# Performance work log

Measured on AMD Instinct MI355X. Metric: run time of the kernel, lower is better.

## Reference

```python
import jax, jax.numpy as jnp
import numpy as np


def setup_inputs() -> dict:
    key = jax.random.key(0)
    k1, k2, k3 = jax.random.split(key, 3)
    B, D, C = 512, 256, 1000
    embedding = jax.random.normal(k1, (B, D), dtype=jnp.float32)
    labels = jax.random.randint(k2, (B,), 0, C, dtype=jnp.int64)
    W = jax.random.normal(k3, (C, D), dtype=jnp.float32) * 0.02
    return {"embedding": embedding, "labels": labels, "W": W}


def reference(embedding, labels, W):
    # MRL-E loss: (1/D) * sum_{k=1..D} CE(z[:, :k] @ W[:, :k].T, y)
    # Computed incrementally: logits_k = logits_{k-1} + z[:, k] outer W[:, k],
    # which is mathematically identical to recomputing the prefix matmul.
    B, D = embedding.shape
    C = W.shape[0]
    rows = jnp.arange(B)
    labels = labels.astype(jnp.int32)

    def step(logits, cols):
        z_col, w_col = cols  # [B], [C]
        logits = logits + z_col[:, None] * w_col[None, :]  # rank-1 update, [B, C]
        # stable cross-entropy: mean(logsumexp(logits) - logits[i, y_i])
        lse = jax.nn.logsumexp(logits, axis=-1)  # [B]
        lab_logit = logits[rows, labels]  # [B]
        loss_k = jnp.mean(lse - lab_logit)
        return logits, loss_k

    init = jnp.zeros((B, C), dtype=embedding.dtype)
    _, losses = jax.lax.scan(step, init, (embedding.T, W.T))  # losses: [D]
    return jnp.sum(losses) / D
```

## Files before the change

### kernel.cpp

```cpp
#include <hip/hip_runtime.h>
#include <hip/hip_bf16.h>
#include <math.h>


#define MRLE_B 512
#define MRLE_D 256
#define MRLE_C 1000
#define MRLE_CP 1024
#define MRLE_KROWS 264
#define MRLE_NT 256
#define LOG2E 1.4426950408889634f
#define LN2   0.6931471805599453f

#if __has_builtin(__builtin_amdgcn_exp2f)
#define EXP2(x) __builtin_amdgcn_exp2f(x)
#else
#define EXP2(x) __builtin_exp2f(x)
#endif

__global__ __launch_bounds__(256) void mrle_transpose(
    const float* __restrict__ W, unsigned short* __restrict__ Wtb)
{
    __shared__ float tile[64][65];
    const int c0 = blockIdx.x * 64;
    const int k0 = blockIdx.y * 64;
    const int t  = threadIdx.x;
    const int r  = t >> 2;
    const int q  = t & 3;

#pragma unroll
    for (int j = 0; j < 4; ++j) {
        const int c    = c0 + r;
        const int kcol = q * 4 + j * 16;
        float4 v = make_float4(0.f, 0.f, 0.f, 0.f);
        if (c < MRLE_C) v = *(const float4*)&W[(size_t)c * MRLE_D + k0 + kcol];
        tile[r][kcol + 0] = v.x;
        tile[r][kcol + 1] = v.y;
        tile[r][kcol + 2] = v.z;
        tile[r][kcol + 3] = v.w;
    }
    __syncthreads();

#pragma unroll
    for (int j = 0; j < 4; ++j) {
        const int cc = q * 4 + j * 16;
        unsigned short hh[4];
#pragma unroll
        for (int e = 0; e < 4; ++e) {
            const float f = tile[cc + e][r] * LOG2E;
            unsigned int u = __float_as_uint(f);
            u = (u + 0x7FFFu + ((u >> 16) & 1u)) >> 16;
            hh[e] = (unsigned short)u;
        }
        *(ushort4*)&Wtb[(size_t)(k0 + r) * MRLE_CP + c0 + cc] =
            make_ushort4(hh[0], hh[1], hh[2], hh[3]);
    }
}

__global__ __launch_bounds__(MRLE_NT) void mrle_main(
    const float* __restrict__ z,
    const int* __restrict__ labels,
    const float* __restrict__ W,
    const unsigned short* __restrict__ Wtb,
    float* __restrict__ out)
{
    __shared__ float zsh[MRLE_D];
    __shared__ float red[4 * 16 * 64];
    __shared__ float Sw[4 * MRLE_D];
    __shared__ float wred[4];

    const int i  = blockIdx.x;
    const int t  = threadIdx.x;
    const int wv = t >> 6;
    const int l  = t & 63;

    zsh[t] = z[i * MRLE_D + t];
    __syncthreads();

    const float ninf = (t < 250) ? 0.f : -INFINITY;
    float l0 = ninf, l1 = ninf, l2 = ninf, l3 = ninf;

    const uint2* Wp2 = (const uint2*)Wtb + t;

    uint2 wbuf[8];
#pragma unroll
    for (int q = 0; q < 8; ++q) wbuf[q] = Wp2[q * (MRLE_CP / 4)];

    float* redw = red + wv * (16 * 64);
    const int khat = l & 15;
    const int q16  = l & 48;

#pragma unroll 1
    for (int cb = 0; cb < 16; ++cb) {
#pragma unroll
        for (int kk = 0; kk < 16; ++kk) {
            const int k = cb * 16 + kk;
            const uint2 w = wbuf[kk & 7];
            const float zk = zsh[k];
            const float w0 = __uint_as_float(w.x << 16);
            const float w1 = __uint_as_float(w.x & 0xFFFF0000u);
            const float w2 = __uint_as_float(w.y << 16);
            const float w3 = __uint_as_float(w.y & 0xFFFF0000u);
            l0 = fmaf(zk, w0, l0);
            l1 = fmaf(zk, w1, l1);
            l2 = fmaf(zk, w2, l2);
            l3 = fmaf(zk, w3, l3);
            redw[kk * 64 + ((l + kk) & 63)] =
                (EXP2(l0) + EXP2(l1)) + (EXP2(l2) + EXP2(l3));
            wbuf[kk & 7] = Wp2[(k + 8) * (MRLE_CP / 4)];
        }

        float s = 0.f;
#pragma unroll
        for (int u = 0; u < 16; ++u)
            s += redw[khat * 64 + ((q16 + u + khat) & 63)];
        s += __shfl_xor(s, 16);
        s += __shfl_xor(s, 32);
        if (l < 16) Sw[wv * MRLE_D + cb * 16 + khat] = s;
    }

    __syncthreads();

    const float S = (Sw[t] + Sw[MRLE_D + t]) +
                    (Sw[2 * MRLE_D + t] + Sw[3 * MRLE_D + t]);
    const float lse2 = __log2f(S);

    const int y = labels[i];
    const float lab = zsh[t] * W[(size_t)y * MRLE_D + t] * (float)(MRLE_D - t);

    float v = lse2 * LN2 - lab;
#pragma unroll
    for (int d = 1; d < 64; d <<= 1) v += __shfl_xor(v, d);
    if (l == 0) wred[wv] = v;
    __syncthreads();
    if (t == 0)
        atomicAdd(out, (wred[0] + wred[1] + wred[2] + wred[3]) *
                           (1.0f / ((float)MRLE_B * (float)MRLE_D)));
}

extern "C" void kernel_launch(void* const* d_in, const int* in_sizes, int n_in,
                              void* d_out, int out_size, void* d_ws, size_t ws_size,
                              hipStream_t stream) {
    const float* z      = (const float*)d_in[0];
    const int*   labels = (const int*)d_in[1];
    const float* W      = (const float*)d_in[2];
    float*       out    = (float*)d_out;

    unsigned short* Wtb = (unsigned short*)d_ws;

    hipMemsetAsync(out, 0, sizeof(float), stream);
    mrle_transpose<<<dim3(16, 4), 256, 0, stream>>>(W, Wtb);
    mrle_main<<<MRLE_B, MRLE_NT, 0, stream>>>(z, labels, W, Wtb, out);
}
```

Baseline: 38.95 us.

## Split class dimension across two blocks per row and add finish kernel

The main kernel now launches two blocks per batch row, each covering half the classes with two columns per thread instead of four. Partial sum-of-exp values per prefix length go to workspace, and a new finish kernel combines them, takes the log, subtracts the label term and reduces. z is read straight from global memory instead of being staged in shared memory. This doubles the number of blocks for more occupancy and latency hiding, at the cost of an extra kernel launch, a workspace round trip, and duplicated loop overhead.

Measured after the change: 45.32 us. +16.3%, slower.

```diff
diff --git a/kernel.cpp b/kernel.cpp
--- a/kernel.cpp
+++ b/kernel.cpp
@@ -9,6 +9,7 @@
 #define MRLE_CP 1024
 #define MRLE_KROWS 264
 #define MRLE_NT 256
+#define ROWD (MRLE_CP / 2)
 #define LOG2E 1.4426950408889634f
 #define LN2   0.6931471805599453f
 
@@ -59,32 +60,30 @@
 
 __global__ __launch_bounds__(MRLE_NT) void mrle_main(
     const float* __restrict__ z,
-    const int* __restrict__ labels,
-    const float* __restrict__ W,
     const unsigned short* __restrict__ Wtb,
-    float* __restrict__ out)
+    float* __restrict__ Sp)
 {
-    __shared__ float zsh[MRLE_D];
     __shared__ float red[4 * 16 * 64];
     __shared__ float Sw[4 * MRLE_D];
-    __shared__ float wred[4];
 
-    const int i  = blockIdx.x;
-    const int t  = threadIdx.x;
-    const int wv = t >> 6;
-    const int l  = t & 63;
+    const int bid = blockIdx.x;
+    const int i   = bid >> 1;
+    const int hc  = bid & 1;
+    const int t   = threadIdx.x;
+    const int wv  = t >> 6;
+    const int l   = t & 63;
 
-    zsh[t] = z[i * MRLE_D + t];
-    __syncthreads();
+    const float* zrow = z + (size_t)i * MRLE_D;
 
-    const float ninf = (t < 250) ? 0.f : -INFINITY;
-    float l0 = ninf, l1 = ninf, l2 = ninf, l3 = ninf;
+    const int cbase = hc * 512 + 2 * t;
+    float l0 = (cbase     < MRLE_C) ? 0.f : -INFINITY;
+    float l1 = (cbase + 1 < MRLE_C) ? 0.f : -INFINITY;
 
-    const uint2* Wp2 = (const uint2*)Wtb + t;
+    const unsigned int* Wp = (const unsigned int*)Wtb + hc * 256 + t;
 
-    uint2 wbuf[8];
+    unsigned int wbuf[8];
 #pragma unroll
-    for (int q = 0; q < 8; ++q) wbuf[q] = Wp2[q * (MRLE_CP / 4)];
+    for (int q = 0; q < 8; ++q) wbuf[q] = Wp[(size_t)q * ROWD];
 
     float* redw = red + wv * (16 * 64);
     const int khat = l & 15;
@@ -95,19 +94,14 @@
 #pragma unroll
         for (int kk = 0; kk < 16; ++kk) {
             const int k = cb * 16 + kk;
-            const uint2 w = wbuf[kk & 7];
-            const float zk = zsh[k];
-            const float w0 = __uint_as_float(w.x << 16);
-            const float w1 = __uint_as_float(w.x & 0xFFFF0000u);
-            const float w2 = __uint_as_float(w.y << 16);
-            const float w3 = __uint_as_float(w.y & 0xFFFF0000u);
+            const unsigned int w = wbuf[kk & 7];
+            const float zk = zrow[k];
+            const float w0 = __uint_as_float(w << 16);
+            const float w1 = __uint_as_float(w & 0xFFFF0000u);
             l0 = fmaf(zk, w0, l0);
             l1 = fmaf(zk, w1, l1);
-            l2 = fmaf(zk, w2, l2);
-            l3 = fmaf(zk, w3, l3);
-            redw[kk * 64 + ((l + kk) & 63)] =
-                (EXP2(l0) + EXP2(l1)) + (EXP2(l2) + EXP2(l3));
-            wbuf[kk & 7] = Wp2[(k + 8) * (MRLE_CP / 4)];
+            redw[kk * 64 + ((l + kk) & 63)] = EXP2(l0) + EXP2(l1);
+            wbuf[kk & 7] = Wp[(size_t)(k + 8) * ROWD];
         }
 
         float s = 0.f;
@@ -121,17 +115,34 @@
 
     __syncthreads();
 
-    const float S = (Sw[t] + Sw[MRLE_D + t]) +
-                    (Sw[2 * MRLE_D + t] + Sw[3 * MRLE_D + t]);
-    const float lse2 = __log2f(S);
+    const float S4 = (Sw[t] + Sw[MRLE_D + t]) +
+                     (Sw[2 * MRLE_D + t] + Sw[3 * MRLE_D + t]);
+    Sp[((size_t)hc * MRLE_B + i) * MRLE_D + t] = S4;
+}
+
+__global__ __launch_bounds__(MRLE_NT) void mrle_finish(
+    const float* __restrict__ Sp,
+    const float* __restrict__ z,
+    const int* __restrict__ labels,
+    const float* __restrict__ W,
+    float* __restrict__ out)
+{
+    __shared__ float wred[4];
+    const int i = blockIdx.x;
+    const int t = threadIdx.x;
+
+    const float s0 = Sp[(size_t)i * MRLE_D + t];
+    const float s1 = Sp[((size_t)MRLE_B + i) * MRLE_D + t];
+    const float lse = LN2 * __log2f(s0 + s1);
 
     const int y = labels[i];
-    const float lab = zsh[t] * W[(size_t)y * MRLE_D + t] * (float)(MRLE_D - t);
+    const float lab = z[i * MRLE_D + t] * W[(size_t)y * MRLE_D + t] *
+                      (float)(MRLE_D - t);
 
-    float v = lse2 * LN2 - lab;
+    float v = lse - lab;
 #pragma unroll
     for (int d = 1; d < 64; d <<= 1) v += __shfl_xor(v, d);
-    if (l == 0) wred[wv] = v;
+    if ((t & 63) == 0) wred[t >> 6] = v;
     __syncthreads();
     if (t == 0)
         atomicAdd(out, (wred[0] + wred[1] + wred[2] + wred[3]) *
@@ -147,8 +158,10 @@
     float*       out    = (float*)d_out;
 
     unsigned short* Wtb = (unsigned short*)d_ws;
+    float*          Sp  = (float*)((char*)d_ws + 544 * 1024);
 
     hipMemsetAsync(out, 0, sizeof(float), stream);
     mrle_transpose<<<dim3(16, 4), 256, 0, stream>>>(W, Wtb);
-    mrle_main<<<MRLE_B, MRLE_NT, 0, stream>>>(z, labels, W, Wtb, out);
+    mrle_main<<<MRLE_B * 2, MRLE_NT, 0, stream>>>(z, Wtb, Sp);
+    mrle_finish<<<MRLE_B, MRLE_NT, 0, stream>>>(Sp, z, labels, W, out);
 }
```

## Use 512 threads per row with two classes per thread

Applied to the files above, without the earlier changes.

Doubles the block size to 512 threads so each thread owns two classes instead of four. This halves the per-thread serial FMA and exp2 chain and adds more waves per block to hide latency. The z values for each 16-step chunk are now loaded from shared memory as float4 vectors into registers. In exchange the per-block shared memory doubles, the reduction covers eight waves, and the stores into the shared reduction buffer happen twice as often per class.

Result: no change. 39.37 us (+1.1%).

```diff
diff --git a/kernel.cpp b/kernel.cpp
--- a/kernel.cpp
+++ b/kernel.cpp
@@ -8,7 +8,8 @@
 #define MRLE_C 1000
 #define MRLE_CP 1024
 #define MRLE_KROWS 264
-#define MRLE_NT 256
+#define MRLE_NT 512
+#define ROWD (MRLE_CP / 2)
 #define LOG2E 1.4426950408889634f
 #define LN2   0.6931471805599453f
 
@@ -65,26 +66,27 @@
     float* __restrict__ out)
 {
     __shared__ float zsh[MRLE_D];
-    __shared__ float red[4 * 16 * 64];
-    __shared__ float Sw[4 * MRLE_D];
-    __shared__ float wred[4];
+    __shared__ float red[8 * 16 * 64];
+    __shared__ float Sw[8 * MRLE_D];
+    __shared__ float wred[8];
 
     const int i  = blockIdx.x;
     const int t  = threadIdx.x;
     const int wv = t >> 6;
     const int l  = t & 63;
 
-    zsh[t] = z[i * MRLE_D + t];
+    if (t < MRLE_D) zsh[t] = z[i * MRLE_D + t];
     __syncthreads();
 
-    const float ninf = (t < 250) ? 0.f : -INFINITY;
-    float l0 = ninf, l1 = ninf, l2 = ninf, l3 = ninf;
+    const int cbase = 2 * t;
+    float l0 = (cbase     < MRLE_C) ? 0.f : -INFINITY;
+    float l1 = (cbase + 1 < MRLE_C) ? 0.f : -INFINITY;
 
-    const uint2* Wp2 = (const uint2*)Wtb + t;
+    const unsigned int* Wp = (const unsigned int*)Wtb + t;
 
-    uint2 wbuf[8];
+    unsigned int wbuf[8];
 #pragma unroll
-    for (int q = 0; q < 8; ++q) wbuf[q] = Wp2[q * (MRLE_CP / 4)];
+    for (int q = 0; q < 8; ++q) wbuf[q] = Wp[(size_t)q * ROWD];
 
     float* redw = red + wv * (16 * 64);
     const int khat = l & 15;
@@ -92,22 +94,22 @@
 
 #pragma unroll 1
     for (int cb = 0; cb < 16; ++cb) {
+        float zq[16];
+        *(float4*)&zq[0]  = *(const float4*)&zsh[cb * 16 + 0];
+        *(float4*)&zq[4]  = *(const float4*)&zsh[cb * 16 + 4];
+        *(float4*)&zq[8]  = *(const float4*)&zsh[cb * 16 + 8];
+        *(float4*)&zq[12] = *(const float4*)&zsh[cb * 16 + 12];
+
 #pragma unroll
         for (int kk = 0; kk < 16; ++kk) {
             const int k = cb * 16 + kk;
-            const uint2 w = wbuf[kk & 7];
-            const float zk = zsh[k];
-            const float w0 = __uint_as_float(w.x << 16);
-            const float w1 = __uint_as_float(w.x & 0xFFFF0000u);
-            const float w2 = __uint_as_float(w.y << 16);
-            const float w3 = __uint_as_float(w.y & 0xFFFF0000u);
-            l0 = fmaf(zk, w0, l0);
-            l1 = fmaf(zk, w1, l1);
-            l2 = fmaf(zk, w2, l2);
-            l3 = fmaf(zk, w3, l3);
-            redw[kk * 64 + ((l + kk) & 63)] =
-                (EXP2(l0) + EXP2(l1)) + (EXP2(l2) + EXP2(l3));
-            wbuf[kk & 7] = Wp2[(k + 8) * (MRLE_CP / 4)];
+            const unsigned int w = wbuf[kk & 7];
+            const float w0 = __uint_as_float(w << 16);
+            const float w1 = __uint_as_float(w & 0xFFFF0000u);
+            l0 = fmaf(zq[kk], w0, l0);
+            l1 = fmaf(zq[kk], w1, l1);
+            redw[kk * 64 + ((l + kk) & 63)] = EXP2(l0) + EXP2(l1);
+            wbuf[kk & 7] = Wp[(size_t)(k + 8) * ROWD];
         }
 
         float s = 0.f;
@@ -121,21 +123,29 @@
 
     __syncthreads();
 
-    const float S = (Sw[t] + Sw[MRLE_D + t]) +
-                    (Sw[2 * MRLE_D + t] + Sw[3 * MRLE_D + t]);
-    const float lse2 = __log2f(S);
+    float v = 0.f;
+    if (t < MRLE_D) {
+        float S = 0.f;
+#pragma unroll
+        for (int wq = 0; wq < 8; ++wq) S += Sw[wq * MRLE_D + t];
+        const float lse = LN2 * __log2f(S);
 
-    const int y = labels[i];
-    const float lab = zsh[t] * W[(size_t)y * MRLE_D + t] * (float)(MRLE_D - t);
+        const int y = labels[i];
+        const float lab = zsh[t] * W[(size_t)y * MRLE_D + t] *
+                          (float)(MRLE_D - t);
+        v = lse - lab;
+    }
 
-    float v = lse2 * LN2 - lab;
 #pragma unroll
     for (int d = 1; d < 64; d <<= 1) v += __shfl_xor(v, d);
     if (l == 0) wred[wv] = v;
     __syncthreads();
-    if (t == 0)
-        atomicAdd(out, (wred[0] + wred[1] + wred[2] + wred[3]) *
-                           (1.0f / ((float)MRLE_B * (float)MRLE_D)));
+    if (t == 0) {
+        float tot = 0.f;
+#pragma unroll
+        for (int wq = 0; wq < 8; ++wq) tot += wred[wq];
+        atomicAdd(out, tot * (1.0f / ((float)MRLE_B * (float)MRLE_D)));
+    }
 }
 
 extern "C" void kernel_launch(void* const* d_in, const int* in_sizes, int n_in,
```
